# Optimization experiments

Hardware: AMD Instinct MI355X
Metric: run time of the kernel (lower is better)

## Reference

```python
import jax, jax.numpy as jnp
import numpy as np
from jax import lax

H = 32  # hidden size (hardcoded in the torch module)

def setup_inputs() -> dict:
    key = jax.random.key(0)
    ks = jax.random.split(key, 7)
    B, T, I = 2048, 512, 64
    s = 1.0 / np.sqrt(H)  # torch nn.LSTM default init scale
    return {
        "x": jax.random.normal(ks[0], (B, T, I), dtype=jnp.float32),
        "W_ih": jax.random.uniform(ks[1], (4 * H, I), jnp.float32, -s, s),
        "W_hh": jax.random.uniform(ks[2], (4 * H, H), jnp.float32, -s, s),
        "b_ih": jax.random.uniform(ks[3], (4 * H,), jnp.float32, -s, s),
        "b_hh": jax.random.uniform(ks[4], (4 * H,), jnp.float32, -s, s),
        "W_fc": jax.random.uniform(ks[5], (1, H), jnp.float32, -s, s),
        "b_fc": jax.random.uniform(ks[6], (1,), jnp.float32, -s, s),
    }

def _lstm_last_h(x, W_ih, W_hh, b_ih, b_hh):
    B = x.shape[0]
    # Precompute input projections for all timesteps: [B, T, 4H] -> [T, B, 4H]
    xg = jnp.einsum('bti,gi->btg', x, W_ih) + (b_ih + b_hh)
    xg = jnp.transpose(xg, (1, 0, 2))

    def step(carry, xt):
        h, c = carry
        g = xt + h @ W_hh.T  # [B, 4H]
        i = jax.nn.sigmoid(g[:, 0 * H:1 * H])
        f = jax.nn.sigmoid(g[:, 1 * H:2 * H])
        gg = jnp.tanh(g[:, 2 * H:3 * H])
        o = jax.nn.sigmoid(g[:, 3 * H:4 * H])
        c = f * c + i * gg
        h = o * jnp.tanh(c)
        return (h, c), None

    init = (jnp.zeros((B, H), x.dtype), jnp.zeros((B, H), x.dtype))
    (h, _), _ = lax.scan(step, init, xg)
    return h  # [B, H], last timestep hidden state

def reference(x, W_ih, W_hh, b_ih, b_hh, W_fc, b_fc):
    # Dropout is identity in eval mode; only the last timestep feeds fc.
    h = _lstm_last_h(x, W_ih, W_hh, b_ih, b_hh)
    return h @ W_fc.T + b_fc  # [B, 1]
```

## Files before the change

### kernel.cpp

```cpp
#include <hip/hip_runtime.h>

typedef __attribute__((ext_vector_type(8))) short short8;
typedef __attribute__((ext_vector_type(4))) float f32x4;

#define LOG2E 1.44269504088896340736f
#define SC1 (-LOG2E)
#define SC2 (-2.0f * LOG2E)

__device__ __forceinline__ unsigned pkcvt(float lo, float hi) {
    unsigned r;
    asm("v_cvt_pk_bf16_f32 %0, %1, %2" : "=v"(r) : "v"(lo), "v"(hi));
    return r;
}
__device__ __forceinline__ float sige(float xpre) {
    return __builtin_amdgcn_rcpf(1.0f + __builtin_amdgcn_exp2f(xpre));
}

__global__ __launch_bounds__(256, 2) void lstm_fused(
    const float* __restrict__ x,
    const float* __restrict__ Wih,
    const float* __restrict__ Whh,
    const float* __restrict__ bih,
    const float* __restrict__ bhh,
    const float* __restrict__ Wfc,
    const float* __restrict__ bfc,
    float* __restrict__ out)
{
    __shared__ unsigned short Wlds[128 * 80];
    __shared__ float xg_sh[4 * 16 * 132];

    const int tid  = threadIdx.x;
    const int lane = tid & 63;
    const int wv   = tid >> 6;
    const int b0   = blockIdx.x * 4 + wv;
    const int m    = lane & 15;
    const int quad = lane >> 4;
    const int cc   = lane & 31;

    {
        const float4* w4 = (const float4*)Wih;
        unsigned* wl = (unsigned*)Wlds;
        #pragma unroll
        for (int i = 0; i < 8; i++) {
            int fi = tid * 8 + i;
            int g  = fi >> 4;
            int k  = (fi & 15) << 2;
            const float s = ((g >> 5) == 2) ? SC2 : SC1;
            float4 v = w4[fi];
            wl[g * 40 + (k >> 1) + 0] = pkcvt(v.x * s, v.y * s);
            wl[g * 40 + (k >> 1) + 1] = pkcvt(v.z * s, v.w * s);
        }
    }

    short8 Bh[8];
    #pragma unroll
    for (int t = 0; t < 8; t++) {
        const float s = ((t >> 1) == 2) ? SC2 : SC1;
        const float4* wr = (const float4*)(Whh + (size_t)(16 * t + m) * 32 + quad * 8);
        float4 va = wr[0], vb = wr[1];
        union { short8 v; unsigned u[4]; } B;
        B.u[0] = pkcvt(va.x * s, va.y * s); B.u[1] = pkcvt(va.z * s, va.w * s);
        B.u[2] = pkcvt(vb.x * s, vb.y * s); B.u[3] = pkcvt(vb.z * s, vb.w * s);
        Bh[t] = B.v;
    }

    f32x4 Cb[8];
    #pragma unroll
    for (int n = 0; n < 8; n++) {
        const float s = ((n >> 1) == 2) ? SC2 : SC1;
        const float b = s * (bih[16 * n + m] + bhh[16 * n + m]);
        Cb[n][0] = b; Cb[n][1] = b; Cb[n][2] = b; Cb[n][3] = b;
    }

    const bool b4  = (lane & 16) != 0;
    const bool odd = (lane & 1) != 0;
    const int badr = quad * 32;

    __syncthreads();

    const float* xrow = x + ((size_t)b0 * 512 + m) * 64;
    float* xgw = xg_sh + wv * 2112;

    float c = 0.0f, h = 0.0f;
    const f32x4 z4 = {0.f, 0.f, 0.f, 0.f};

    float4 p0, p1, p2, p3;
    {
        const float4* r0 = (const float4*)xrow;
        p0 = r0[quad * 2];     p1 = r0[quad * 2 + 1];
        p2 = r0[8 + quad * 2]; p3 = r0[8 + quad * 2 + 1];
    }

    for (int ch = 0; ch < 32; ++ch) {
        union { short8 v; unsigned u[4]; } A0, A1;
        A0.u[0] = pkcvt(p0.x, p0.y); A0.u[1] = pkcvt(p0.z, p0.w);
        A0.u[2] = pkcvt(p1.x, p1.y); A0.u[3] = pkcvt(p1.z, p1.w);
        A1.u[0] = pkcvt(p2.x, p2.y); A1.u[1] = pkcvt(p2.z, p2.w);
        A1.u[2] = pkcvt(p3.x, p3.y); A1.u[3] = pkcvt(p3.z, p3.w);

        {
            const int chn = (ch < 31) ? ch + 1 : 31;
            const float4* n0 = (const float4*)(xrow + (size_t)chn * 1024);
            p0 = n0[quad * 2];     p1 = n0[quad * 2 + 1];
            p2 = n0[8 + quad * 2]; p3 = n0[8 + quad * 2 + 1];
        }

        #pragma unroll
        for (int n = 0; n < 8; n++) {
            const short8 B0 = *(const short8*)&Wlds[(16 * n + m) * 80 + quad * 8];
            const short8 B1 = *(const short8*)&Wlds[(16 * n + m) * 80 + 32 + quad * 8];
            f32x4 ar0 = __builtin_amdgcn_mfma_f32_16x16x32_bf16(A0.v, B0, Cb[n], 0, 0, 0);
            ar0       = __builtin_amdgcn_mfma_f32_16x16x32_bf16(A1.v, B1, ar0,   0, 0, 0);
            const int pos = ((n & 1) << 6) + 4 * m + (n >> 1);
            #pragma unroll
            for (int r = 0; r < 4; r++) {
                xgw[(quad * 4 + r) * 132 + pos] = ar0[r];
            }
        }

        #pragma unroll
        for (int tt = 0; tt < 16; ++tt) {
            union { float f; int i; } hu; hu.f = h;
            union { int i; float f; } hxu;
            hxu.i = __builtin_amdgcn_mov_dpp(hu.i, 0xB1, 0xF, 0xF, true);
            const unsigned pe = pkcvt(h, hxu.f);
            const unsigned po = pkcvt(hxu.f, h);
            const int pair = odd ? (int)po : (int)pe;

            union { short8 v; int u[4]; } abf;
            abf.u[0] = __builtin_amdgcn_ds_bpermute(badr,      pair);
            abf.u[1] = __builtin_amdgcn_ds_bpermute(badr + 8,  pair);
            abf.u[2] = __builtin_amdgcn_ds_bpermute(badr + 16, pair);
            abf.u[3] = __builtin_amdgcn_ds_bpermute(badr + 24, pair);

            const f32x4 a0 = __builtin_amdgcn_mfma_f32_16x16x32_bf16(abf.v, Bh[0], z4, 0, 0, 0);
            const f32x4 a1 = __builtin_amdgcn_mfma_f32_16x16x32_bf16(abf.v, Bh[1], z4, 0, 0, 0);
            const f32x4 a2 = __builtin_amdgcn_mfma_f32_16x16x32_bf16(abf.v, Bh[2], z4, 0, 0, 0);
            const f32x4 a3 = __builtin_amdgcn_mfma_f32_16x16x32_bf16(abf.v, Bh[3], z4, 0, 0, 0);
            const f32x4 a4 = __builtin_amdgcn_mfma_f32_16x16x32_bf16(abf.v, Bh[4], z4, 0, 0, 0);
            const f32x4 a5 = __builtin_amdgcn_mfma_f32_16x16x32_bf16(abf.v, Bh[5], z4, 0, 0, 0);
            const f32x4 a6 = __builtin_amdgcn_mfma_f32_16x16x32_bf16(abf.v, Bh[6], z4, 0, 0, 0);
            const f32x4 a7 = __builtin_amdgcn_mfma_f32_16x16x32_bf16(abf.v, Bh[7], z4, 0, 0, 0);
            const float hi = b4 ? a1[0] : a0[0];
            const float hf = b4 ? a3[0] : a2[0];
            const float hg = b4 ? a5[0] : a4[0];
            const float ho = b4 ? a7[0] : a6[0];

            const f32x4 xg4 = *(const f32x4*)&xgw[tt * 132 + 4 * cc];
            const float iv = sige(xg4[0] + hi);
            const float fv = sige(xg4[1] + hf);
            const float gv = fmaf(2.0f, sige(xg4[2] + hg), -1.0f);
            const float ov = sige(xg4[3] + ho);
            c = fmaf(fv, c, iv * gv);
            const float th = fmaf(2.0f, sige(c * SC2), -1.0f);
            h = ov * th;
        }
    }

    float p = h * Wfc[cc];
    #pragma unroll
    for (int msk = 16; msk >= 1; msk >>= 1) p += __shfl_xor(p, msk);
    if (lane == 0) out[b0] = p + bfc[0];
}

extern "C" void kernel_launch(void* const* d_in, const int* in_sizes, int n_in,
                              void* d_out, int out_size, void* d_ws, size_t ws_size,
                              hipStream_t stream) {
    const float* x   = (const float*)d_in[0];
    const float* Wih = (const float*)d_in[1];
    const float* Whh = (const float*)d_in[2];
    const float* bih = (const float*)d_in[3];
    const float* bhh = (const float*)d_in[4];
    const float* Wfc = (const float*)d_in[5];
    const float* bfc = (const float*)d_in[6];
    float* out = (float*)d_out;
    lstm_fused<<<dim3(512), dim3(256), 0, stream>>>(x, Wih, Whh, bih, bhh, Wfc, bfc, out);
}
```

Measured before the change: 433.9 us.

## Split gate activations across wave halves and exchange h through LDS

The four gate sigmoids per hidden unit are now split across the two 32-lane halves of the wavefront. Each lane computes two sigmoids, then uses permlane32_swap to fetch the partner half's values, which halves the transcendental work per lane. The h vector for the next step's MFMA is written to a small per-wave LDS buffer as bf16 and read back as a short8, replacing the DPP plus four ds_bpermute gather. The xg layout is reshuffled to match. This relies on wave-local LDS ordering without an explicit barrier and on permlane32_swap support on gfx950.

```diff
diff --git a/kernel.cpp b/kernel.cpp
--- a/kernel.cpp
+++ b/kernel.cpp
@@ -15,6 +15,8 @@
 __device__ __forceinline__ float sige(float xpre) {
     return __builtin_amdgcn_rcpf(1.0f + __builtin_amdgcn_exp2f(xpre));
 }
+__device__ __forceinline__ unsigned f2u(float f) { union { float f; unsigned u; } v; v.f = f; return v.u; }
+__device__ __forceinline__ float u2f(unsigned u) { union { unsigned u; float f; } v; v.u = u; return v.f; }
 
 __global__ __launch_bounds__(256, 2) void lstm_fused(
     const float* __restrict__ x,
@@ -28,6 +30,7 @@
 {
     __shared__ unsigned short Wlds[128 * 80];
     __shared__ float xg_sh[4 * 16 * 132];
+    __shared__ alignas(64) unsigned short hbuf[4 * 64];
 
     const int tid  = threadIdx.x;
     const int lane = tid & 63;
@@ -72,15 +75,23 @@
         Cb[n][0] = b; Cb[n][1] = b; Cb[n][2] = b; Cb[n][3] = b;
     }
 
-    const bool b4  = (lane & 16) != 0;
-    const bool odd = (lane & 1) != 0;
-    const int badr = quad * 32;
+    const bool b4    = (lane & 16) != 0;
+    const bool upper = (lane & 32) != 0;
+
+    bool x_lo;
+    {
+        const unsigned probe = upper ? 1u : 0u;
+        auto dr = __builtin_amdgcn_permlane32_swap(probe, probe, false, false);
+        x_lo = (dr[0] == 0u);
+    }
 
     __syncthreads();
 
     const float* xrow = x + ((size_t)b0 * 512 + m) * 64;
     float* xgw = xg_sh + wv * 2112;
+    unsigned short* hw = hbuf + wv * 64;
 
+    hw[lane] = 0;
     float c = 0.0f, h = 0.0f;
     const f32x4 z4 = {0.f, 0.f, 0.f, 0.f};
 
@@ -111,49 +122,48 @@
             const short8 B1 = *(const short8*)&Wlds[(16 * n + m) * 80 + 32 + quad * 8];
             f32x4 ar0 = __builtin_amdgcn_mfma_f32_16x16x32_bf16(A0.v, B0, Cb[n], 0, 0, 0);
             ar0       = __builtin_amdgcn_mfma_f32_16x16x32_bf16(A1.v, B1, ar0,   0, 0, 0);
-            const int pos = ((n & 1) << 6) + 4 * m + (n >> 1);
+            const int so = 2 * m + 32 * (n & 1) + 64 * (n >> 2) + ((n >> 1) & 1);
             #pragma unroll
             for (int r = 0; r < 4; r++) {
-                xgw[(quad * 4 + r) * 132 + pos] = ar0[r];
+                xgw[(quad * 4 + r) * 132 + so] = ar0[r];
             }
         }
 
         #pragma unroll
         for (int tt = 0; tt < 16; ++tt) {
-            union { float f; int i; } hu; hu.f = h;
-            union { int i; float f; } hxu;
-            hxu.i = __builtin_amdgcn_mov_dpp(hu.i, 0xB1, 0xF, 0xF, true);
-            const unsigned pe = pkcvt(h, hxu.f);
-            const unsigned po = pkcvt(hxu.f, h);
-            const int pair = odd ? (int)po : (int)pe;
+            const short8 abf = *(const short8*)&hw[quad * 8];
+            const f32x4 a0 = __builtin_amdgcn_mfma_f32_16x16x32_bf16(abf, Bh[0], z4, 0, 0, 0);
+            const f32x4 a1 = __builtin_amdgcn_mfma_f32_16x16x32_bf16(abf, Bh[1], z4, 0, 0, 0);
+            const f32x4 a4 = __builtin_amdgcn_mfma_f32_16x16x32_bf16(abf, Bh[4], z4, 0, 0, 0);
+            const f32x4 a5 = __builtin_amdgcn_mfma_f32_16x16x32_bf16(abf, Bh[5], z4, 0, 0, 0);
+            const f32x4 a2 = __builtin_amdgcn_mfma_f32_16x16x32_bf16(abf, Bh[2], z4, 0, 0, 0);
+            const f32x4 a3 = __builtin_amdgcn_mfma_f32_16x16x32_bf16(abf, Bh[3], z4, 0, 0, 0);
+            const f32x4 a6 = __builtin_amdgcn_mfma_f32_16x16x32_bf16(abf, Bh[6], z4, 0, 0, 0);
+            const f32x4 a7 = __builtin_amdgcn_mfma_f32_16x16x32_bf16(abf, Bh[7], z4, 0, 0, 0);
 
-            union { short8 v; int u[4]; } abf;
-            abf.u[0] = __builtin_amdgcn_ds_bpermute(badr,      pair);
-            abf.u[1] = __builtin_amdgcn_ds_bpermute(badr + 8,  pair);
-            abf.u[2] = __builtin_amdgcn_ds_bpermute(badr + 16, pair);
-            abf.u[3] = __builtin_amdgcn_ds_bpermute(badr + 24, pair);
+            const float gaL = b4 ? a1[0] : a0[0];
+            const float gaU = b4 ? a5[0] : a4[0];
+            const float gbL = b4 ? a3[0] : a2[0];
+            const float gbU = b4 ? a7[0] : a6[0];
+            const float hA  = upper ? gaU : gaL;
+            const float hB  = upper ? gbU : gbL;
 
-            const f32x4 a0 = __builtin_amdgcn_mfma_f32_16x16x32_bf16(abf.v, Bh[0], z4, 0, 0, 0);
-            const f32x4 a1 = __builtin_amdgcn_mfma_f32_16x16x32_bf16(abf.v, Bh[1], z4, 0, 0, 0);
-            const f32x4 a2 = __builtin_amdgcn_mfma_f32_16x16x32_bf16(abf.v, Bh[2], z4, 0, 0, 0);
-            const f32x4 a3 = __builtin_amdgcn_mfma_f32_16x16x32_bf16(abf.v, Bh[3], z4, 0, 0, 0);
-            const f32x4 a4 = __builtin_amdgcn_mfma_f32_16x16x32_bf16(abf.v, Bh[4], z4, 0, 0, 0);
-            const f32x4 a5 = __builtin_amdgcn_mfma_f32_16x16x32_bf16(abf.v, Bh[5], z4, 0, 0, 0);
-            const f32x4 a6 = __builtin_amdgcn_mfma_f32_16x16x32_bf16(abf.v, Bh[6], z4, 0, 0, 0);
-            const f32x4 a7 = __builtin_amdgcn_mfma_f32_16x16x32_bf16(abf.v, Bh[7], z4, 0, 0, 0);
-            const float hi = b4 ? a1[0] : a0[0];
-            const float hf = b4 ? a3[0] : a2[0];
-            const float hg = b4 ? a5[0] : a4[0];
-            const float ho = b4 ? a7[0] : a6[0];
+            const float2 xg2 = *(const float2*)&xgw[tt * 132 + 2 * lane];
+            const float s1 = sige(xg2.x + hA);
+            const float s2 = sige(xg2.y + hB);
 
-            const f32x4 xg4 = *(const f32x4*)&xgw[tt * 132 + 4 * cc];
-            const float iv = sige(xg4[0] + hi);
-            const float fv = sige(xg4[1] + hf);
-            const float gv = fmaf(2.0f, sige(xg4[2] + hg), -1.0f);
-            const float ov = sige(xg4[3] + ho);
+            auto r1 = __builtin_amdgcn_permlane32_swap(f2u(s1), f2u(s1), false, false);
+            const float iv  = u2f(x_lo ? r1[0] : r1[1]);
+            const float gvr = u2f(x_lo ? r1[1] : r1[0]);
+            auto r2 = __builtin_amdgcn_permlane32_swap(f2u(s2), f2u(s2), false, false);
+            const float fv = u2f(x_lo ? r2[0] : r2[1]);
+            const float ov = u2f(x_lo ? r2[1] : r2[0]);
+
+            const float gv = fmaf(2.0f, gvr, -1.0f);
             c = fmaf(fv, c, iv * gv);
-            const float th = fmaf(2.0f, sige(c * SC2), -1.0f);
-            h = ov * th;
+            const float th = sige(c * SC2);
+            h = fmaf(ov + ov, th, -ov);
+            hw[lane] = (unsigned short)pkcvt(h, h);
         }
     }
 
```

Result: no change. 429.5 us (-1.0%).
